# Performance work log

Hardware: AMD Instinct MI355X
Metric: run time of the kernel (lower is better)

The kernel has to match this reference:

```python
import jax, jax.numpy as jnp
import numpy as np
from jax import lax

S, B, F = 512, 256, 128
HC = 256  # constraint LSTM hidden
HG = 256  # generation LSTM hidden
L = 128   # linear units


def _lstm_step(Wih, Whh, bias):
    """torch.nn.LSTMCell semantics: gates = x@Wih.T + h@Whh.T + bih + bhh,
    chunked as (i, f, g, o)."""
    def step(carry, x):
        h, c = carry
        gates = x @ Wih.T + h @ Whh.T + bias
        i, f, g, o = jnp.split(gates, 4, axis=-1)
        c2 = jax.nn.sigmoid(f) * c + jax.nn.sigmoid(i) * jnp.tanh(g)
        h2 = jax.nn.sigmoid(o) * jnp.tanh(c2)
        return (h2, c2), h2
    return step


def setup_inputs() -> dict:
    key = jax.random.key(0)
    ks = jax.random.split(key, 16)
    s = 0.05
    return {
        "seq": jax.random.normal(ks[0], (S, B, F), jnp.float32),
        "seq_constraints": jax.random.normal(ks[1], (S, B, F + 1), jnp.float32),
        "Wih_c": jax.random.normal(ks[2], (4 * HC, F + 1), jnp.float32) * s,
        "Whh_c": jax.random.normal(ks[3], (4 * HC, HC), jnp.float32) * s,
        "bih_c": jax.random.normal(ks[4], (4 * HC,), jnp.float32) * s,
        "bhh_c": jax.random.normal(ks[5], (4 * HC,), jnp.float32) * s,
        "Wih_g": jax.random.normal(ks[6], (4 * HG, F + HC), jnp.float32) * s,
        "Whh_g": jax.random.normal(ks[7], (4 * HG, HG), jnp.float32) * s,
        "bih_g": jax.random.normal(ks[8], (4 * HG,), jnp.float32) * s,
        "bhh_g": jax.random.normal(ks[9], (4 * HG,), jnp.float32) * s,
        "W1": jax.random.normal(ks[10], (L, HG), jnp.float32) * s,
        "b1": jax.random.normal(ks[11], (L,), jnp.float32) * s,
        "W2": jax.random.normal(ks[12], (F, L), jnp.float32) * s,
        "b2": jax.random.normal(ks[13], (F,), jnp.float32) * s,
    }


def reference(seq, seq_constraints, Wih_c, Whh_c, bih_c, bhh_c,
              Wih_g, Whh_g, bih_g, bhh_g, W1, b1, W2, b2):
    seq_len, batch, nf = seq.shape
    dt = seq.dtype

    # --- constraint LSTM, scanned backward in time; outputs aligned to time index ---
    step_c = _lstm_step(Wih_c, Whh_c, bih_c + bhh_c)
    z_c = jnp.zeros((batch, HC), dt)
    _, hc = lax.scan(step_c, (z_c, z_c), seq_constraints, reverse=True)  # (S,B,HC)

    # --- generation LSTM input: seq shifted right by one step (zeros at t=0),
    #     concatenated with the constraint hidden at time t ---
    shifted = jnp.concatenate([jnp.zeros((1, batch, nf), dt), seq[:-1]], axis=0)
    gen_in = jnp.concatenate([shifted, hc], axis=-1)  # (S,B,F+HC)

    step_g = _lstm_step(Wih_g, Whh_g, bih_g + bhh_g)
    z_g = jnp.zeros((batch, HG), dt)
    _, hg = lax.scan(step_g, (z_g, z_g), gen_in)  # (S,B,HG)

    # --- per-step MLP head ---
    preds = jax.nn.relu(hg @ W1.T + b1) @ W2.T + b2  # (S,B,F)
    return preds
```

## Files before the change

kernel.cpp:

```cpp
#include <hip/hip_runtime.h>

typedef unsigned short u16;
typedef unsigned int u32;
typedef unsigned long long u64;
typedef __attribute__((ext_vector_type(8))) short s16x8;
typedef __attribute__((ext_vector_type(4))) float f32x4;

#define MFMA_BF16 __builtin_amdgcn_mfma_f32_16x16x32_bf16

#define TCH 64
#define NCH 8
#define CROWS (TCH * 256)

__device__ __forceinline__ float b2f(u16 u) {
  u32 v = ((u32)u) << 16; float f; __builtin_memcpy(&f, &v, 4); return f;
}
__device__ __forceinline__ u16 f2b(float f) {
  u32 u; __builtin_memcpy(&u, &f, 4);
  u += 0x7FFFu + ((u >> 16) & 1u);
  return (u16)(u >> 16);
}
__device__ __forceinline__ float sigm(float x) {
  float e = __builtin_amdgcn_exp2f(-1.44269504f * x);
  return __builtin_amdgcn_rcpf(1.0f + e);
}
__device__ __forceinline__ float tanh_(float x) {
  float e = __builtin_amdgcn_exp2f(2.88539008f * x);
  return 1.0f - 2.0f * __builtin_amdgcn_rcpf(e + 1.0f);
}

__global__ void prep_weights(const float* __restrict__ Wihc, const float* __restrict__ Whhc,
                             const float* __restrict__ bihc, const float* __restrict__ bhhc,
                             const float* __restrict__ Wihg, const float* __restrict__ Whhg,
                             const float* __restrict__ bihg, const float* __restrict__ bhhg,
                             const float* __restrict__ W1, const float* __restrict__ W2,
                             u16* __restrict__ pWihc, u16* __restrict__ pWhhc,
                             u16* __restrict__ pWihg, u16* __restrict__ pWhhg,
                             u16* __restrict__ pW1, u16* __restrict__ pW2,
                             float* __restrict__ pbc, float* __restrict__ pbg) {
  const int b = blockIdx.x, t = threadIdx.x;
  if (b < 1024) { if (t < 192) pWihc[b * 192 + t] = (t < 129) ? f2b(Wihc[b * 129 + t]) : (u16)0; }
  else if (b < 2048) { int n = b - 1024; pWhhc[n * 256 + t] = f2b(Whhc[n * 256 + t]); }
  else if (b < 3072) { int n = b - 2048; for (int k = t; k < 384; k += 256) pWihg[n * 384 + k] = f2b(Wihg[n * 384 + k]); }
  else if (b < 4096) { int n = b - 3072; pWhhg[n * 256 + t] = f2b(Whhg[n * 256 + t]); }
  else if (b < 4224) { int n = b - 4096; pW1[n * 256 + t] = f2b(W1[n * 256 + t]); }
  else if (b < 4352) { int n = b - 4224; if (t < 128) pW2[n * 128 + t] = f2b(W2[n * 128 + t]); }
  else {
    int i = (b - 4352) * 256 + t;
    if (i < 1024) pbc[i] = bihc[i] + bhhc[i];
    else if (i < 2048) pbg[i - 1024] = bihg[i - 1024] + bhhg[i - 1024];
  }
}

__global__ void fill_val(float* __restrict__ p, float v, int n) {
  int i = blockIdx.x * 256 + threadIdx.x;
  if (i < n) p[i] = v;
}

template <int MODE>
__device__ __forceinline__ void gate_gemm_tile(
    int tile, int r0, const float* __restrict__ F, const u16* __restrict__ Hb,
    const u16* __restrict__ Bw, const float* __restrict__ bias,
    u16* __restrict__ Out, u16* Al, u16* Bl) {
  const int K = (MODE == 1) ? 192 : 384;
  const int bm = tile >> 3, bn = tile & 7;
  const int m0 = bm << 7, n0 = bn << 7;
  const int tid = threadIdx.x, lane = tid & 63, w = tid >> 6;
  const int kg = lane >> 4, l15 = lane & 15;
  const int mq = (w & 1) << 6, nq = (w >> 1) << 6;

  f32x4 acc[4][4];
#pragma unroll
  for (int mt = 0; mt < 4; ++mt)
#pragma unroll
    for (int nt = 0; nt < 4; ++nt) acc[mt][nt] = (f32x4){0.f, 0.f, 0.f, 0.f};

#pragma unroll 1
  for (int kc = 0; kc < K; kc += 64) {
#pragma unroll
    for (int i = 0; i < 4; ++i) {
      int id = i * 256 + tid;
      int row = id >> 3;
      int c8 = (id & 7) * 8;
      int k = kc + c8;
      s16x8 av;
      if (MODE == 1) {
        const float* s = F + (size_t)(r0 + m0 + row) * 129 + k;
#pragma unroll
        for (int j = 0; j < 8; ++j) {
          u16 bb = 0;
          if (k + j < 129) bb = f2b(s[j]);
          av[j] = (short)bb;
        }
      } else {
        if (k < 128) {
          const int grow = r0 + m0 + row;
          if (grow < 256) {
            av = (s16x8){0, 0, 0, 0, 0, 0, 0, 0};
          } else {
            const float* s = F + (size_t)(grow - 256) * 128 + k;
#pragma unroll
            for (int j = 0; j < 8; ++j) av[j] = (short)f2b(s[j]);
          }
        } else {
          av = *(const s16x8*)&Hb[(size_t)(m0 + row) * 256 + (k - 128)];
        }
      }
      s16x8 bv = *(const s16x8*)(Bw + (size_t)(n0 + row) * K + k);
      int sw = (row & 7) << 3;
      *(s16x8*)&Al[row * 64 + (c8 ^ sw)] = av;
      *(s16x8*)&Bl[row * 64 + (c8 ^ sw)] = bv;
    }
    __syncthreads();
#pragma unroll
    for (int kk = 0; kk < 2; ++kk) {
      const int kb = kk * 32 + kg * 8;
      s16x8 a[4], b[4];
#pragma unroll
      for (int mt = 0; mt < 4; ++mt) {
        int r = mq + mt * 16 + l15;
        a[mt] = *(const s16x8*)&Al[r * 64 + (kb ^ ((r & 7) << 3))];
      }
#pragma unroll
      for (int nt = 0; nt < 4; ++nt) {
        int r = nq + nt * 16 + l15;
        b[nt] = *(const s16x8*)&Bl[r * 64 + (kb ^ ((r & 7) << 3))];
      }
#pragma unroll
      for (int mt = 0; mt < 4; ++mt)
#pragma unroll
        for (int nt = 0; nt < 4; ++nt)
          acc[mt][nt] = MFMA_BF16(a[mt], b[nt], acc[mt][nt], 0, 0, 0);
    }
    __syncthreads();
  }
#pragma unroll
  for (int nt = 0; nt < 4; ++nt) {
    const int col = n0 + nq + nt * 16 + l15;
    const float bb = bias[col];
#pragma unroll
    for (int mt = 0; mt < 4; ++mt)
#pragma unroll
      for (int r = 0; r < 4; ++r) {
        const size_t orow = (size_t)(m0 + mq + mt * 16 + kg * 4 + r);
        Out[orow * 1024 + col] = f2b(acc[mt][nt][r] + bb);
      }
  }
}

template <int MODE>
__global__ __launch_bounds__(256, 1) void gate_gemm_k(
    int r0, const float* __restrict__ F, const u16* __restrict__ Hb,
    const u16* __restrict__ Bw, const float* __restrict__ bias,
    u16* __restrict__ Out) {
  __shared__ u16 Al[8192], Bl[8192];
  gate_gemm_tile<MODE>(blockIdx.x, r0, F, Hb, Bw, bias, Out, Al, Bl);
}

template <int RELU, int OUTF32>
__device__ __forceinline__ void head_tile(
    int tile, const u16* __restrict__ A, int lda,
    const u16* __restrict__ Bw, const float* __restrict__ bias,
    void* __restrict__ Outv, u16* Al, u16* Bl) {
  const int m0 = tile << 7;
  const int tid = threadIdx.x, lane = tid & 63, w = tid >> 6;
  const int kg = lane >> 4, l15 = lane & 15;
  const int mq = (w & 1) << 6, nq = (w >> 1) << 6;

  f32x4 acc[4][4];
#pragma unroll
  for (int mt = 0; mt < 4; ++mt)
#pragma unroll
    for (int nt = 0; nt < 4; ++nt) acc[mt][nt] = (f32x4){0.f, 0.f, 0.f, 0.f};

#pragma unroll 1
  for (int kc = 0; kc < lda; kc += 64) {
#pragma unroll
    for (int i = 0; i < 4; ++i) {
      int id = i * 256 + tid;
      int row = id >> 3;
      int c8 = (id & 7) * 8;
      int k = kc + c8;
      s16x8 av = *(const s16x8*)(A + (size_t)(m0 + row) * lda + k);
      s16x8 bv = *(const s16x8*)(Bw + (size_t)row * lda + k);
      int sw = (row & 7) << 3;
      *(s16x8*)&Al[row * 64 + (c8 ^ sw)] = av;
      *(s16x8*)&Bl[row * 64 + (c8 ^ sw)] = bv;
    }
    __syncthreads();
#pragma unroll
    for (int kk = 0; kk < 2; ++kk) {
      const int kb = kk * 32 + kg * 8;
      s16x8 a[4], b[4];
#pragma unroll
      for (int mt = 0; mt < 4; ++mt) {
        int r = mq + mt * 16 + l15;
        a[mt] = *(const s16x8*)&Al[r * 64 + (kb ^ ((r & 7) << 3))];
      }
#pragma unroll
      for (int nt = 0; nt < 4; ++nt) {
        int r = nq + nt * 16 + l15;
        b[nt] = *(const s16x8*)&Bl[r * 64 + (kb ^ ((r & 7) << 3))];
      }
#pragma unroll
      for (int mt = 0; mt < 4; ++mt)
#pragma unroll
        for (int nt = 0; nt < 4; ++nt)
          acc[mt][nt] = MFMA_BF16(a[mt], b[nt], acc[mt][nt], 0, 0, 0);
    }
    __syncthreads();
  }
#pragma unroll
  for (int nt = 0; nt < 4; ++nt) {
    const int col = nq + nt * 16 + l15;
    const float bb = bias[col];
#pragma unroll
    for (int mt = 0; mt < 4; ++mt)
#pragma unroll
      for (int r = 0; r < 4; ++r) {
        float v = acc[mt][nt][r] + bb;
        if (RELU) v = fmaxf(v, 0.f);
        const size_t orow = (size_t)(m0 + mq + mt * 16 + kg * 4 + r);
        if (OUTF32) ((float*)Outv)[orow * 128 + col] = v;
        else ((u16*)Outv)[orow * 128 + col] = f2b(v);
      }
  }
}

template <int RELU, int OUTF32>
__global__ __launch_bounds__(256, 1) void head_k(
    const u16* __restrict__ A, int lda, const u16* __restrict__ Bw,
    const float* __restrict__ bias, void* __restrict__ Outv) {
  __shared__ u16 Al[8192], Bl[8192];
  head_tile<RELU, OUTF32>(blockIdx.x, A, lda, Bw, bias, Outv, Al, Bl);
}

template <int GMODE>
__global__ __launch_bounds__(256, 1) void lstm_scan(
    const u16* __restrict__ X, const u16* __restrict__ Whh,
    u16* __restrict__ Hc, const u16* __restrict__ ph,
    float* __restrict__ Cst, u64* __restrict__ HX, u32* __restrict__ slots,
    int base, int fwd, int first,
    const float* __restrict__ gF, const u16* __restrict__ gHb,
    const u16* __restrict__ gBw, const float* __restrict__ gbias,
    u16* __restrict__ gOut, int gr0, int ng,
    const u16* __restrict__ h1A, u16* __restrict__ h1Out, int nh1,
    const u16* __restrict__ h2A, float* __restrict__ h2Out, int nh2,
    const u16* __restrict__ W1b, const float* __restrict__ b1,
    const u16* __restrict__ W2b, const float* __restrict__ b2) {
  __shared__ u16 lds[16384];
  int bx = blockIdx.x;
  if (bx >= 64) {
    bx -= 64;
    if (bx < ng) { gate_gemm_tile<GMODE>(bx, gr0, gF, gHb, gBw, gbias, gOut, lds, lds + 8192); return; }
    bx -= ng;
    if (bx < nh1) { head_tile<1, 0>(bx, h1A, 256, W1b, b1, (void*)h1Out, lds, lds + 8192); return; }
    bx -= nh1;
    if (bx < nh2) { head_tile<0, 1>(bx, h2A, 128, W2b, b2, (void*)h2Out, lds, lds + 8192); }
    return;
  }
  __builtin_amdgcn_s_setprio(1);
  u16* hlds = lds;

  const int tid = threadIdx.x;
  const int lane = tid & 63;
  const int w = tid >> 6;
  const int bg = blockIdx.x & 7;
  const int hs = blockIdx.x >> 3;
  const int kg = lane >> 4;
  const int l15 = lane & 15;
  const int mrow = (w & 1) * 16;
  const int rowL = mrow + l15;
  const int brow = bg * 32 + rowL;
  const int hcol0 = hs * 32 + (w >> 1) * 16 + kg * 4;
  u32* myslot = slots + ((bg << 3) + hs) * 32 + w;

  s16x8 breg[4][8];
  const int wrow = hs * 32 + (w >> 1) * 16 + l15;
#pragma unroll
  for (int q = 0; q < 4; ++q)
#pragma unroll
    for (int kt = 0; kt < 8; ++kt)
      breg[q][kt] = *(const s16x8*)&Whh[(size_t)(q * 256 + wrow) * 256 + kt * 32 + kg * 8];

  if (first) {
#pragma unroll
    for (int i = 0; i < 8; ++i) {
      int idx = i * 256 + tid;
      int row = idx >> 6, c0 = (idx & 63) * 4;
      *(u64*)&hlds[row * 256 + (c0 ^ ((row & 7) << 3))] = 0ull;
    }
  } else {
    const u64* hsrc = (const u64*)ph + bg * 2048;
#pragma unroll
    for (int i = 0; i < 8; ++i) {
      int idx = i * 256 + tid;
      int row = idx >> 6, c0 = (idx & 63) * 4;
      u64 v = hsrc[idx];
      *(u64*)&hlds[row * 256 + (c0 ^ ((row & 7) << 3))] = v;
    }
  }
  float c4[4];
  if (first) {
    c4[0] = 0.f; c4[1] = 0.f; c4[2] = 0.f; c4[3] = 0.f;
  } else {
    f32x4 cv = *(const f32x4*)&Cst[(size_t)brow * 256 + hcol0];
    c4[0] = cv[0]; c4[1] = cv[1]; c4[2] = cv[2]; c4[3] = cv[3];
  }
  __syncthreads();

  u64 xv[4];
  {
    const int lt0 = fwd ? 0 : TCH - 1;
    const u16* xb = X + ((size_t)lt0 * 256 + brow) * 1024 + hcol0;
#pragma unroll
    for (int q = 0; q < 4; ++q) xv[q] = *(const u64*)(xb + q * 256);
  }

  const int abase = rowL * 256;
  const int aswz = (rowL & 7) << 3;
  const int widx = (w >> 1) * 4 + kg;
  const int rrow = tid >> 3;
  const int ridx = tid & 7;

#pragma unroll 1
  for (int s = 0; s < TCH; ++s) {
    const int lt = fwd ? s : TCH - 1 - s;
    const u32 tag = (u32)(base + s + 1);
    u64* slab = HX + ((size_t)(s & 1) * 8 + bg) * 2048;

    f32x4 acc[2][4];
#pragma unroll
    for (int p = 0; p < 2; ++p)
#pragma unroll
      for (int q = 0; q < 4; ++q) acc[p][q] = (f32x4){0.f, 0.f, 0.f, 0.f};

#pragma unroll
    for (int kt = 0; kt < 8; ++kt) {
      s16x8 hb = *(const s16x8*)&hlds[abase + ((kt * 32 + kg * 8) ^ aswz)];
#pragma unroll
      for (int q = 0; q < 4; ++q)
        acc[kt & 1][q] = MFMA_BF16(breg[q][kt], hb, acc[kt & 1][q], 0, 0, 0);
    }

    u64 hu = 0;
#pragma unroll
    for (int r = 0; r < 4; ++r) {
      float gi = acc[0][0][r] + acc[1][0][r] + b2f((u16)(xv[0] >> (16 * r)));
      float gf = acc[0][1][r] + acc[1][1][r] + b2f((u16)(xv[1] >> (16 * r)));
      float gg = acc[0][2][r] + acc[1][2][r] + b2f((u16)(xv[2] >> (16 * r)));
      float go = acc[0][3][r] + acc[1][3][r] + b2f((u16)(xv[3] >> (16 * r)));
      float cn = sigm(gf) * c4[r] + sigm(gi) * tanh_(gg);
      c4[r] = cn;
      hu |= ((u64)f2b(sigm(go) * tanh_(cn))) << (16 * r);
    }

    *(u64*)&Hc[((size_t)lt * 256 + brow) * 256 + hcol0] = hu;
    if (s == TCH - 1) break;
    __hip_atomic_store(slab + ((size_t)hs * 32 + rowL) * 8 + widx, hu,
                       __ATOMIC_RELAXED, __HIP_MEMORY_SCOPE_AGENT);

    __builtin_amdgcn_sched_barrier(0);
    asm volatile("s_waitcnt vmcnt(0)" ::: "memory");
    __builtin_amdgcn_sched_barrier(0);
    if (lane == 0)
      __hip_atomic_store(myslot, tag, __ATOMIC_RELAXED, __HIP_MEMORY_SCOPE_AGENT);

    {
      const int nlt = fwd ? lt + 1 : lt - 1;
      const u16* xb = X + ((size_t)nlt * 256 + brow) * 1024 + hcol0;
#pragma unroll
      for (int q = 0; q < 4; ++q) xv[q] = *(const u64*)(xb + q * 256);
    }
    __builtin_amdgcn_sched_barrier(0);

    if (w == 0 && lane < 32) {
      const u32* sp = slots + ((bg << 3) + (lane >> 2)) * 32 + (lane & 3);
      int guard = 0;
      while (__hip_atomic_load(sp, __ATOMIC_RELAXED, __HIP_MEMORY_SCOPE_AGENT) < tag &&
             guard < (1 << 15)) {
        __builtin_amdgcn_s_sleep(1);
        ++guard;
      }
    }
    __builtin_amdgcn_s_barrier();

    u64 pv[8];
#pragma unroll
    for (int k = 0; k < 8; ++k)
      pv[k] = __hip_atomic_load(slab + k * 256 + tid,
                                __ATOMIC_RELAXED, __HIP_MEMORY_SCOPE_AGENT);
#pragma unroll
    for (int k = 0; k < 8; ++k) {
      int c = k * 32 + ridx * 4;
      *(u64*)&hlds[rrow * 256 + (c ^ ((rrow & 7) << 3))] = pv[k];
    }
    __syncthreads();
  }

  f32x4 cv; cv[0] = c4[0]; cv[1] = c4[1]; cv[2] = c4[2]; cv[3] = c4[3];
  *(f32x4*)&Cst[(size_t)brow * 256 + hcol0] = cv;
}

extern "C" void kernel_launch(void* const* d_in, const int* in_sizes, int n_in,
                              void* d_out, int out_size, void* d_ws, size_t ws_size,
                              hipStream_t stream) {
  (void)in_sizes; (void)n_in;
  const float* seq  = (const float*)d_in[0];
  const float* sc   = (const float*)d_in[1];
  const float* Wihc = (const float*)d_in[2];
  const float* Whhc = (const float*)d_in[3];
  const float* bihc = (const float*)d_in[4];
  const float* bhhc = (const float*)d_in[5];
  const float* Wihg = (const float*)d_in[6];
  const float* Whhg = (const float*)d_in[7];
  const float* bihg = (const float*)d_in[8];
  const float* bhhg = (const float*)d_in[9];
  const float* W1   = (const float*)d_in[10];
  const float* b1   = (const float*)d_in[11];
  const float* W2   = (const float*)d_in[12];
  const float* b2   = (const float*)d_in[13];

  const size_t XB = (size_t)CROWS * 1024 * 2;
  const size_t HGB = (size_t)CROWS * 256 * 2;
  const size_t T1B = (size_t)CROWS * 128 * 2;
  const size_t TAILB = 1024 * 192 * 2 + 1024 * 256 * 2 + 1024 * 384 * 2 +
                       1024 * 256 * 2 + 128 * 256 * 2 + 128 * 128 * 2 +
                       1024 * 4 + 1024 * 4 + 256 * 256 * 4 +
                       (size_t)2 * 8 * 2048 * 8 + 64 * 128;
  const size_t NEED_BIG = 2 * XB + 2 * HGB + 2 * T1B + TAILB;
  const size_t NEED_SMALL = XB + HGB + T1B + TAILB;
  const int use2 = ws_size >= NEED_BIG;

  if (ws_size < NEED_SMALL) {
    fill_val<<<(out_size + 255) / 256, 256, 0, stream>>>((float*)d_out, 1.0e6f, out_size);
    return;
  }

  char* ws = (char*)d_ws;
  size_t off = 0;
  u16* Xh[2]; u16* hgb[2]; u16* t1b[2];
  Xh[0] = (u16*)(ws + off); off += XB;
  Xh[1] = use2 ? (u16*)(ws + off) : Xh[0]; if (use2) off += XB;
  hgb[0] = (u16*)(ws + off); off += HGB;
  hgb[1] = use2 ? (u16*)(ws + off) : hgb[0]; if (use2) off += HGB;
  t1b[0] = (u16*)(ws + off); off += T1B;
  t1b[1] = use2 ? (u16*)(ws + off) : t1b[0]; if (use2) off += T1B;
  u16* pWihc = (u16*)(ws + off); off += 1024 * 192 * 2;
  u16* pWhhc = (u16*)(ws + off); off += 1024 * 256 * 2;
  u16* pWihg = (u16*)(ws + off); off += 1024 * 384 * 2;
  u16* pWhhg = (u16*)(ws + off); off += 1024 * 256 * 2;
  u16* pW1   = (u16*)(ws + off); off += 128 * 256 * 2;
  u16* pW2   = (u16*)(ws + off); off += 128 * 128 * 2;
  float* pbc = (float*)(ws + off); off += 1024 * 4;
  float* pbg = (float*)(ws + off); off += 1024 * 4;
  float* Cst = (float*)(ws + off); off += 256 * 256 * 4;
  u64* HX    = (u64*)(ws + off); off += (size_t)2 * 8 * 2048 * 8;
  u32* slots = (u32*)(ws + off);

  u16* hcb = (u16*)d_out;
  float* outf = (float*)d_out;

  hipMemsetAsync(slots, 0, 64 * 128, stream);
  prep_weights<<<4360, 256, 0, stream>>>(Wihc, Whhc, bihc, bhhc, Wihg, Whhg, bihg, bhhg,
                                         W1, W2, pWihc, pWhhc, pWihg, pWhhg, pW1, pW2, pbc, pbg);

  if (use2) {
    gate_gemm_k<1><<<1024, 256, 0, stream>>>(7 * CROWS, sc, (const u16*)0, pWihc, pbc, Xh[1]);
    for (int c = NCH - 1; c >= 0; --c) {
      const int ord = NCH - 1 - c;
      const int ng = (c > 0) ? 1024 : 0;
      u16* Hcp = hcb + (size_t)c * TCH * 65536;
      const u16* ph = (c == NCH - 1) ? (const u16*)0 : hcb + (size_t)(c + 1) * TCH * 65536;
      lstm_scan<1><<<64 + ng, 256, 0, stream>>>(
          Xh[c & 1], pWhhc, Hcp, ph, Cst, HX, slots, ord * TCH, 0, c == NCH - 1,
          sc, (const u16*)0, pWihc, pbc, Xh[(c - 1) & 1], (c - 1) * CROWS, ng,
          (const u16*)0, (u16*)0, 0, (const u16*)0, (float*)0, 0, pW1, b1, pW2, b2);
    }
    gate_gemm_k<2><<<1024, 256, 0, stream>>>(0, seq, hcb, pWihg, pbg, Xh[0]);
    for (int c = 0; c < NCH; ++c) {
      const int ord = NCH + c;
      const int ng = (c < NCH - 1) ? 1024 : 0;
      const int nh1 = (c >= 1) ? 128 : 0;
      const int nh2 = (c >= 2) ? 128 : 0;
      const u16* ph = (c == 0) ? (const u16*)0 : hgb[(c - 1) & 1] + (size_t)(TCH - 1) * 65536;
      lstm_scan<2><<<64 + ng + nh1 + nh2, 256, 0, stream>>>(
          Xh[c & 1], pWhhg, hgb[c & 1], ph, Cst, HX, slots, ord * TCH, 1, c == 0,
          seq, hcb + (size_t)(c + 1) * TCH * 65536, pWihg, pbg,
          Xh[(c + 1) & 1], (c + 1) * CROWS, ng,
          hgb[(c - 1) & 1], t1b[(c - 1) & 1], nh1,
          t1b[c & 1], outf + (size_t)(c - 2) * CROWS * 128, nh2,
          pW1, b1, pW2, b2);
    }
    head_k<1, 0><<<128, 256, 0, stream>>>(hgb[1], 256, pW1, b1, (void*)t1b[1]);
    head_k<0, 1><<<128, 256, 0, stream>>>(t1b[0], 128, pW2, b2,
                                          (void*)(outf + (size_t)6 * CROWS * 128));
    head_k<0, 1><<<128, 256, 0, stream>>>(t1b[1], 128, pW2, b2,
                                          (void*)(outf + (size_t)7 * CROWS * 128));
  } else {
    for (int c = NCH - 1; c >= 0; --c) {
      gate_gemm_k<1><<<1024, 256, 0, stream>>>(c * CROWS, sc, (const u16*)0, pWihc, pbc, Xh[0]);
      u16* Hcp = hcb + (size_t)c * TCH * 65536;
      const u16* ph = (c == NCH - 1) ? (const u16*)0 : hcb + (size_t)(c + 1) * TCH * 65536;
      lstm_scan<1><<<64, 256, 0, stream>>>(
          Xh[0], pWhhc, Hcp, ph, Cst, HX, slots, (NCH - 1 - c) * TCH, 0, c == NCH - 1,
          sc, (const u16*)0, pWihc, pbc, Xh[0], 0, 0,
          (const u16*)0, (u16*)0, 0, (const u16*)0, (float*)0, 0, pW1, b1, pW2, b2);
    }
    for (int c = 0; c < NCH; ++c) {
      gate_gemm_k<2><<<1024, 256, 0, stream>>>(c * CROWS, seq,
                                               hcb + (size_t)c * TCH * 65536, pWihg, pbg, Xh[0]);
      const u16* ph = (c == 0) ? (const u16*)0 : hgb[0] + (size_t)(TCH - 1) * 65536;
      lstm_scan<2><<<64, 256, 0, stream>>>(
          Xh[0], pWhhg, hgb[0], ph, Cst, HX, slots, (NCH + c) * TCH, 1, c == 0,
          seq, (const u16*)0, pWihg, pbg, Xh[0], 0, 0,
          (const u16*)0, (u16*)0, 0, (const u16*)0, (float*)0, 0, pW1, b1, pW2, b2);
      head_k<1, 0><<<128, 256, 0, stream>>>(hgb[0], 256, pW1, b1, (void*)t1b[0]);
      head_k<0, 1><<<128, 256, 0, stream>>>(t1b[0], 128, pW2, b2,
                                            (void*)(outf + (size_t)c * CROWS * 128));
    }
  }
}
```

Baseline: 3.346 ms.

## Replace slot-flag handshake with tag-embedded hidden-state exchange and drop fused overlap

Each bf16 hidden value is now packed with the step tag in its own 32-bit word. Readers poll the exchange buffer directly until every tag matches, which replaces the separate slot flags, the vmcnt wait and the sleep-based poll with a single spin on the data. At the same time, the fused launches that ran gate GEMMs and head tiles alongside the scan blocks are removed, along with the double-buffered workspace path, so all stages run serially. The exchange buffer doubles in size, and the change gives up overlap of the input GEMMs and heads with the recurrence.

```diff
diff --git a/kernel.cpp b/kernel.cpp
--- a/kernel.cpp
+++ b/kernel.cpp
@@ -5,6 +5,7 @@
 typedef unsigned long long u64;
 typedef __attribute__((ext_vector_type(8))) short s16x8;
 typedef __attribute__((ext_vector_type(4))) float f32x4;
+typedef __attribute__((ext_vector_type(4))) u32 u32x4;
 
 #define MFMA_BF16 __builtin_amdgcn_mfma_f32_16x16x32_bf16
 
@@ -58,12 +59,13 @@
 }
 
 template <int MODE>
-__device__ __forceinline__ void gate_gemm_tile(
-    int tile, int r0, const float* __restrict__ F, const u16* __restrict__ Hb,
+__global__ __launch_bounds__(256, 1) void gate_gemm_k(
+    int r0, const float* __restrict__ F, const u16* __restrict__ Hb,
     const u16* __restrict__ Bw, const float* __restrict__ bias,
-    u16* __restrict__ Out, u16* Al, u16* Bl) {
+    u16* __restrict__ Out) {
+  __shared__ u16 Al[8192], Bl[8192];
   const int K = (MODE == 1) ? 192 : 384;
-  const int bm = tile >> 3, bn = tile & 7;
+  const int bm = blockIdx.x >> 3, bn = blockIdx.x & 7;
   const int m0 = bm << 7, n0 = bn << 7;
   const int tid = threadIdx.x, lane = tid & 63, w = tid >> 6;
   const int kg = lane >> 4, l15 = lane & 15;
@@ -148,21 +150,12 @@
   }
 }
 
-template <int MODE>
-__global__ __launch_bounds__(256, 1) void gate_gemm_k(
-    int r0, const float* __restrict__ F, const u16* __restrict__ Hb,
-    const u16* __restrict__ Bw, const float* __restrict__ bias,
-    u16* __restrict__ Out) {
+template <int RELU, int OUTF32>
+__global__ __launch_bounds__(256, 1) void head_k(
+    const u16* __restrict__ A, int lda, const u16* __restrict__ Bw,
+    const float* __restrict__ bias, void* __restrict__ Outv) {
   __shared__ u16 Al[8192], Bl[8192];
-  gate_gemm_tile<MODE>(blockIdx.x, r0, F, Hb, Bw, bias, Out, Al, Bl);
-}
-
-template <int RELU, int OUTF32>
-__device__ __forceinline__ void head_tile(
-    int tile, const u16* __restrict__ A, int lda,
-    const u16* __restrict__ Bw, const float* __restrict__ bias,
-    void* __restrict__ Outv, u16* Al, u16* Bl) {
-  const int m0 = tile << 7;
+  const int m0 = blockIdx.x << 7;
   const int tid = threadIdx.x, lane = tid & 63, w = tid >> 6;
   const int kg = lane >> 4, l15 = lane & 15;
   const int mq = (w & 1) << 6, nq = (w >> 1) << 6;
@@ -227,41 +220,12 @@
   }
 }
 
-template <int RELU, int OUTF32>
-__global__ __launch_bounds__(256, 1) void head_k(
-    const u16* __restrict__ A, int lda, const u16* __restrict__ Bw,
-    const float* __restrict__ bias, void* __restrict__ Outv) {
-  __shared__ u16 Al[8192], Bl[8192];
-  head_tile<RELU, OUTF32>(blockIdx.x, A, lda, Bw, bias, Outv, Al, Bl);
-}
-
-template <int GMODE>
 __global__ __launch_bounds__(256, 1) void lstm_scan(
     const u16* __restrict__ X, const u16* __restrict__ Whh,
     u16* __restrict__ Hc, const u16* __restrict__ ph,
-    float* __restrict__ Cst, u64* __restrict__ HX, u32* __restrict__ slots,
-    int base, int fwd, int first,
-    const float* __restrict__ gF, const u16* __restrict__ gHb,
-    const u16* __restrict__ gBw, const float* __restrict__ gbias,
-    u16* __restrict__ gOut, int gr0, int ng,
-    const u16* __restrict__ h1A, u16* __restrict__ h1Out, int nh1,
-    const u16* __restrict__ h2A, float* __restrict__ h2Out, int nh2,
-    const u16* __restrict__ W1b, const float* __restrict__ b1,
-    const u16* __restrict__ W2b, const float* __restrict__ b2) {
-  __shared__ u16 lds[16384];
-  int bx = blockIdx.x;
-  if (bx >= 64) {
-    bx -= 64;
-    if (bx < ng) { gate_gemm_tile<GMODE>(bx, gr0, gF, gHb, gBw, gbias, gOut, lds, lds + 8192); return; }
-    bx -= ng;
-    if (bx < nh1) { head_tile<1, 0>(bx, h1A, 256, W1b, b1, (void*)h1Out, lds, lds + 8192); return; }
-    bx -= nh1;
-    if (bx < nh2) { head_tile<0, 1>(bx, h2A, 128, W2b, b2, (void*)h2Out, lds, lds + 8192); }
-    return;
-  }
-  __builtin_amdgcn_s_setprio(1);
-  u16* hlds = lds;
-
+    float* __restrict__ Cst, u64* __restrict__ HX,
+    int base, int fwd, int first) {
+  __shared__ u16 hlds[32 * 256];
   const int tid = threadIdx.x;
   const int lane = tid & 63;
   const int w = tid >> 6;
@@ -273,7 +237,10 @@
   const int rowL = mrow + l15;
   const int brow = bg * 32 + rowL;
   const int hcol0 = hs * 32 + (w >> 1) * 16 + kg * 4;
-  u32* myslot = slots + ((bg << 3) + hs) * 32 + w;
+
+  const int rrow = tid >> 3;
+  const int rcol0 = (tid & 7) * 32;
+  const int rsw = (rrow & 7) << 3;
 
   s16x8 breg[4][8];
   const int wrow = hs * 32 + (w >> 1) * 16 + l15;
@@ -319,15 +286,13 @@
 
   const int abase = rowL * 256;
   const int aswz = (rowL & 7) << 3;
-  const int widx = (w >> 1) * 4 + kg;
-  const int rrow = tid >> 3;
-  const int ridx = tid & 7;
 
 #pragma unroll 1
   for (int s = 0; s < TCH; ++s) {
     const int lt = fwd ? s : TCH - 1 - s;
     const u32 tag = (u32)(base + s + 1);
-    u64* slab = HX + ((size_t)(s & 1) * 8 + bg) * 2048;
+    const u64 tagpat = (u64)tag * 0x100000001ull;
+    u64* slab = HX + ((size_t)(s & 1) * 8 + bg) * 4096;
 
     f32x4 acc[2][4];
 #pragma unroll
@@ -343,6 +308,7 @@
         acc[kt & 1][q] = MFMA_BF16(breg[q][kt], hb, acc[kt & 1][q], 0, 0, 0);
     }
 
+    u16 hb16[4];
     u64 hu = 0;
 #pragma unroll
     for (int r = 0; r < 4; ++r) {
@@ -352,48 +318,59 @@
       float go = acc[0][3][r] + acc[1][3][r] + b2f((u16)(xv[3] >> (16 * r)));
       float cn = sigm(gf) * c4[r] + sigm(gi) * tanh_(gg);
       c4[r] = cn;
-      hu |= ((u64)f2b(sigm(go) * tanh_(cn))) << (16 * r);
-    }
-
+      hb16[r] = f2b(sigm(go) * tanh_(cn));
+      hu |= ((u64)hb16[r]) << (16 * r);
+    }
+
+    if (s == TCH - 1) {
+      *(u64*)&Hc[((size_t)lt * 256 + brow) * 256 + hcol0] = hu;
+      break;
+    }
+
+    {
+      u64* wp = slab + (size_t)rowL * 128 + (hcol0 >> 1);
+      u64 w0 = (u64)(((u32)hb16[0] << 16) | tag) | ((u64)(((u32)hb16[1] << 16) | tag) << 32);
+      u64 w1 = (u64)(((u32)hb16[2] << 16) | tag) | ((u64)(((u32)hb16[3] << 16) | tag) << 32);
+      __hip_atomic_store(wp + 0, w0, __ATOMIC_RELAXED, __HIP_MEMORY_SCOPE_AGENT);
+      __hip_atomic_store(wp + 1, w1, __ATOMIC_RELAXED, __HIP_MEMORY_SCOPE_AGENT);
+    }
     *(u64*)&Hc[((size_t)lt * 256 + brow) * 256 + hcol0] = hu;
-    if (s == TCH - 1) break;
-    __hip_atomic_store(slab + ((size_t)hs * 32 + rowL) * 8 + widx, hu,
-                       __ATOMIC_RELAXED, __HIP_MEMORY_SCOPE_AGENT);
-
-    __builtin_amdgcn_sched_barrier(0);
-    asm volatile("s_waitcnt vmcnt(0)" ::: "memory");
-    __builtin_amdgcn_sched_barrier(0);
-    if (lane == 0)
-      __hip_atomic_store(myslot, tag, __ATOMIC_RELAXED, __HIP_MEMORY_SCOPE_AGENT);
-
     {
       const int nlt = fwd ? lt + 1 : lt - 1;
       const u16* xb = X + ((size_t)nlt * 256 + brow) * 1024 + hcol0;
 #pragma unroll
       for (int q = 0; q < 4; ++q) xv[q] = *(const u64*)(xb + q * 256);
     }
+    asm volatile("" ::: "memory");
+
+    u64 wv[16];
+    {
+      const u64* rp = slab + (size_t)rrow * 128 + (rcol0 >> 1);
+      int guard = 0;
+      for (;;) {
+#pragma unroll
+        for (int k = 0; k < 16; ++k)
+          wv[k] = __hip_atomic_load(rp + k, __ATOMIC_RELAXED, __HIP_MEMORY_SCOPE_AGENT);
+        u64 bad = 0;
+#pragma unroll
+        for (int k = 0; k < 16; ++k) bad |= (wv[k] ^ tagpat);
+        if ((bad & 0x0000FFFF0000FFFFull) == 0 || ++guard >= (1 << 12)) break;
+      }
+    }
+
+    __builtin_amdgcn_s_barrier();
     __builtin_amdgcn_sched_barrier(0);
 
-    if (w == 0 && lane < 32) {
-      const u32* sp = slots + ((bg << 3) + (lane >> 2)) * 32 + (lane & 3);
-      int guard = 0;
-      while (__hip_atomic_load(sp, __ATOMIC_RELAXED, __HIP_MEMORY_SCOPE_AGENT) < tag &&
-             guard < (1 << 15)) {
-        __builtin_amdgcn_s_sleep(1);
-        ++guard;
-      }
-    }
-    __builtin_amdgcn_s_barrier();
-
-    u64 pv[8];
-#pragma unroll
-    for (int k = 0; k < 8; ++k)
-      pv[k] = __hip_atomic_load(slab + k * 256 + tid,
-                                __ATOMIC_RELAXED, __HIP_MEMORY_SCOPE_AGENT);
-#pragma unroll
-    for (int k = 0; k < 8; ++k) {
-      int c = k * 32 + ridx * 4;
-      *(u64*)&hlds[rrow * 256 + (c ^ ((rrow & 7) << 3))] = pv[k];
+#pragma unroll
+    for (int j = 0; j < 4; ++j) {
+      u32x4 out;
+#pragma unroll
+      for (int i = 0; i < 4; ++i) {
+        u64 v = wv[4 * j + i];
+        out[i] = (((u32)v) >> 16) | ((u32)(v >> 32) & 0xFFFF0000u);
+      }
+      int elem = (rcol0 + 8 * j) ^ rsw;
+      *(u32x4*)&hlds[rrow * 256 + elem] = out;
     }
     __syncthreads();
   }
@@ -421,31 +398,11 @@
   const float* W2   = (const float*)d_in[12];
   const float* b2   = (const float*)d_in[13];
 
-  const size_t XB = (size_t)CROWS * 1024 * 2;
-  const size_t HGB = (size_t)CROWS * 256 * 2;
-  const size_t T1B = (size_t)CROWS * 128 * 2;
-  const size_t TAILB = 1024 * 192 * 2 + 1024 * 256 * 2 + 1024 * 384 * 2 +
-                       1024 * 256 * 2 + 128 * 256 * 2 + 128 * 128 * 2 +
-                       1024 * 4 + 1024 * 4 + 256 * 256 * 4 +
-                       (size_t)2 * 8 * 2048 * 8 + 64 * 128;
-  const size_t NEED_BIG = 2 * XB + 2 * HGB + 2 * T1B + TAILB;
-  const size_t NEED_SMALL = XB + HGB + T1B + TAILB;
-  const int use2 = ws_size >= NEED_BIG;
-
-  if (ws_size < NEED_SMALL) {
-    fill_val<<<(out_size + 255) / 256, 256, 0, stream>>>((float*)d_out, 1.0e6f, out_size);
-    return;
-  }
-
   char* ws = (char*)d_ws;
   size_t off = 0;
-  u16* Xh[2]; u16* hgb[2]; u16* t1b[2];
-  Xh[0] = (u16*)(ws + off); off += XB;
-  Xh[1] = use2 ? (u16*)(ws + off) : Xh[0]; if (use2) off += XB;
-  hgb[0] = (u16*)(ws + off); off += HGB;
-  hgb[1] = use2 ? (u16*)(ws + off) : hgb[0]; if (use2) off += HGB;
-  t1b[0] = (u16*)(ws + off); off += T1B;
-  t1b[1] = use2 ? (u16*)(ws + off) : t1b[0]; if (use2) off += T1B;
+  u16* Xbuf = (u16*)(ws + off); off += (size_t)CROWS * 1024 * 2;
+  u16* hgb  = (u16*)(ws + off); off += (size_t)CROWS * 256 * 2;
+  u16* t1b  = (u16*)(ws + off); off += (size_t)CROWS * 128 * 2;
   u16* pWihc = (u16*)(ws + off); off += 1024 * 192 * 2;
   u16* pWhhc = (u16*)(ws + off); off += 1024 * 256 * 2;
   u16* pWihg = (u16*)(ws + off); off += 1024 * 384 * 2;
@@ -455,69 +412,39 @@
   float* pbc = (float*)(ws + off); off += 1024 * 4;
   float* pbg = (float*)(ws + off); off += 1024 * 4;
   float* Cst = (float*)(ws + off); off += 256 * 256 * 4;
-  u64* HX    = (u64*)(ws + off); off += (size_t)2 * 8 * 2048 * 8;
-  u32* slots = (u32*)(ws + off);
+  u64* HX    = (u64*)(ws + off); off += (size_t)2 * 8 * 4096 * 8;
+  const size_t NEEDED = off;
+
+  if (ws_size < NEEDED) {
+    fill_val<<<(out_size + 255) / 256, 256, 0, stream>>>((float*)d_out, 1.0e6f, out_size);
+    return;
+  }
 
   u16* hcb = (u16*)d_out;
   float* outf = (float*)d_out;
 
-  hipMemsetAsync(slots, 0, 64 * 128, stream);
+  hipMemsetAsync(HX, 0, (size_t)2 * 8 * 4096 * 8, stream);
   prep_weights<<<4360, 256, 0, stream>>>(Wihc, Whhc, bihc, bhhc, Wihg, Whhg, bihg, bhhg,
                                          W1, W2, pWihc, pWhhc, pWihg, pWhhg, pW1, pW2, pbc, pbg);
 
-  if (use2) {
-    gate_gemm_k<1><<<1024, 256, 0, stream>>>(7 * CROWS, sc, (const u16*)0, pWihc, pbc, Xh[1]);
-    for (int c = NCH - 1; c >= 0; --c) {
-      const int ord = NCH - 1 - c;
-      const int ng = (c > 0) ? 1024 : 0;
-      u16* Hcp = hcb + (size_t)c * TCH * 65536;
-      const u16* ph = (c == NCH - 1) ? (const u16*)0 : hcb + (size_t)(c + 1) * TCH * 65536;
-      lstm_scan<1><<<64 + ng, 256, 0, stream>>>(
-          Xh[c & 1], pWhhc, Hcp, ph, Cst, HX, slots, ord * TCH, 0, c == NCH - 1,
-          sc, (const u16*)0, pWihc, pbc, Xh[(c - 1) & 1], (c - 1) * CROWS, ng,
-          (const u16*)0, (u16*)0, 0, (const u16*)0, (float*)0, 0, pW1, b1, pW2, b2);
-    }
-    gate_gemm_k<2><<<1024, 256, 0, stream>>>(0, seq, hcb, pWihg, pbg, Xh[0]);
-    for (int c = 0; c < NCH; ++c) {
-      const int ord = NCH + c;
-      const int ng = (c < NCH - 1) ? 1024 : 0;
-      const int nh1 = (c >= 1) ? 128 : 0;
-      const int nh2 = (c >= 2) ? 128 : 0;
-      const u16* ph = (c == 0) ? (const u16*)0 : hgb[(c - 1) & 1] + (size_t)(TCH - 1) * 65536;
-      lstm_scan<2><<<64 + ng + nh1 + nh2, 256, 0, stream>>>(
-          Xh[c & 1], pWhhg, hgb[c & 1], ph, Cst, HX, slots, ord * TCH, 1, c == 0,
-          seq, hcb + (size_t)(c + 1) * TCH * 65536, pWihg, pbg,
-          Xh[(c + 1) & 1], (c + 1) * CROWS, ng,
-          hgb[(c - 1) & 1], t1b[(c - 1) & 1], nh1,
-          t1b[c & 1], outf + (size_t)(c - 2) * CROWS * 128, nh2,
-          pW1, b1, pW2, b2);
-    }
-    head_k<1, 0><<<128, 256, 0, stream>>>(hgb[1], 256, pW1, b1, (void*)t1b[1]);
-    head_k<0, 1><<<128, 256, 0, stream>>>(t1b[0], 128, pW2, b2,
-                                          (void*)(outf + (size_t)6 * CROWS * 128));
-    head_k<0, 1><<<128, 256, 0, stream>>>(t1b[1], 128, pW2, b2,
-                                          (void*)(outf + (size_t)7 * CROWS * 128));
-  } else {
-    for (int c = NCH - 1; c >= 0; --c) {
-      gate_gemm_k<1><<<1024, 256, 0, stream>>>(c * CROWS, sc, (const u16*)0, pWihc, pbc, Xh[0]);
-      u16* Hcp = hcb + (size_t)c * TCH * 65536;
-      const u16* ph = (c == NCH - 1) ? (const u16*)0 : hcb + (size_t)(c + 1) * TCH * 65536;
-      lstm_scan<1><<<64, 256, 0, stream>>>(
-          Xh[0], pWhhc, Hcp, ph, Cst, HX, slots, (NCH - 1 - c) * TCH, 0, c == NCH - 1,
-          sc, (const u16*)0, pWihc, pbc, Xh[0], 0, 0,
-          (const u16*)0, (u16*)0, 0, (const u16*)0, (float*)0, 0, pW1, b1, pW2, b2);
-    }
-    for (int c = 0; c < NCH; ++c) {
-      gate_gemm_k<2><<<1024, 256, 0, stream>>>(c * CROWS, seq,
-                                               hcb + (size_t)c * TCH * 65536, pWihg, pbg, Xh[0]);
-      const u16* ph = (c == 0) ? (const u16*)0 : hgb[0] + (size_t)(TCH - 1) * 65536;
-      lstm_scan<2><<<64, 256, 0, stream>>>(
-          Xh[0], pWhhg, hgb[0], ph, Cst, HX, slots, (NCH + c) * TCH, 1, c == 0,
-          seq, (const u16*)0, pWihg, pbg, Xh[0], 0, 0,
-          (const u16*)0, (u16*)0, 0, (const u16*)0, (float*)0, 0, pW1, b1, pW2, b2);
-      head_k<1, 0><<<128, 256, 0, stream>>>(hgb[0], 256, pW1, b1, (void*)t1b[0]);
-      head_k<0, 1><<<128, 256, 0, stream>>>(t1b[0], 128, pW2, b2,
-                                            (void*)(outf + (size_t)c * CROWS * 128));
-    }
-  }
-}
+  for (int c = NCH - 1; c >= 0; --c) {
+    gate_gemm_k<1><<<1024, 256, 0, stream>>>(c * CROWS, sc, (const u16*)0, pWihc, pbc, Xbuf);
+    u16* Hcp = hcb + (size_t)c * TCH * 65536;
+    const u16* ph = (c == NCH - 1) ? (const u16*)0 : hcb + (size_t)(c + 1) * TCH * 65536;
+    const int ord = NCH - 1 - c;
+    lstm_scan<<<64, 256, 0, stream>>>(Xbuf, pWhhc, Hcp, ph, Cst, HX,
+                                      ord * TCH, 0, c == NCH - 1);
+  }
+
+  for (int c = 0; c < NCH; ++c) {
+    gate_gemm_k<2><<<1024, 256, 0, stream>>>(c * CROWS, seq,
+                                             hcb + (size_t)c * TCH * 65536, pWihg, pbg, Xbuf);
+    const u16* ph = (c == 0) ? (const u16*)0 : hgb + (size_t)(TCH - 1) * 65536;
+    const int ord = NCH + c;
+    lstm_scan<<<64, 256, 0, stream>>>(Xbuf, pWhhg, hgb, ph, Cst, HX,
+                                      ord * TCH, 1, c == 0);
+    head_k<1, 0><<<128, 256, 0, stream>>>(hgb, 256, pW1, b1, (void*)t1b);
+    head_k<0, 1><<<128, 256, 0, stream>>>(t1b, 128, pW2, b2,
+                                          (void*)(outf + (size_t)c * CROWS * 128));
+  }
+}
```

Result: slower. 7.727 ms (+131.0%).
